# Performance work log

Hardware: AMD Instinct MI355X
Metric: run time of the kernel (lower is better)

The kernel has to match this reference:

```python
import jax, jax.numpy as jnp
import numpy as np

N_EXPERTS = 8
D_MODEL = 1024
D_FF = 2048
NUM_TOKENS = 16384


def setup_inputs() -> dict:
    key = jax.random.key(0)
    k1, k2, k3, k4 = jax.random.split(key, 4)
    x = jax.random.normal(k1, (NUM_TOKENS, D_MODEL), dtype=jnp.float32)
    expert_indices = jax.random.randint(k2, (NUM_TOKENS,), 0, N_EXPERTS, dtype=jnp.int32)
    # init per nn.init.normal_(std=0.02)
    gate_up_weight = 0.02 * jax.random.normal(k3, (N_EXPERTS, 2 * D_FF, D_MODEL), dtype=jnp.float32)
    down_weight = 0.02 * jax.random.normal(k4, (N_EXPERTS, D_MODEL, D_FF), dtype=jnp.float32)
    return {"x": x, "expert_indices": expert_indices,
            "gate_up_weight": gate_up_weight, "down_weight": down_weight}


def reference(x, expert_indices, gate_up_weight, down_weight):
    # Faithful math: each token t uses expert e = expert_indices[t]:
    #   combined = x @ gate_up_weight[e].T ; gate, up = split ; h = silu(gate)*up
    #   out = h @ down_weight[e].T
    # Implemented as a fixed loop over the (small) expert set with masked
    # accumulation, avoiding the original's per-token [2F,D] weight gather.
    n_experts = gate_up_weight.shape[0]
    d_ff = down_weight.shape[2]
    out = jnp.zeros((x.shape[0], down_weight.shape[1]), dtype=x.dtype)
    for e in range(n_experts):
        combined = x @ gate_up_weight[e].T                  # [T, 2*d_ff]
        gate, up = combined[:, :d_ff], combined[:, d_ff:]
        hidden = jax.nn.silu(gate) * up                     # [T, d_ff]
        o = hidden @ down_weight[e].T                       # [T, d_model]
        out = out + jnp.where((expert_indices == e)[:, None], o, 0.0)
    return out
```

## Files before the change

kernel.cpp:

```cpp
#include <hip/hip_runtime.h>

#define NTOK 16384
#define DM 1024
#define DFF 2048
#define NE 8

typedef unsigned short u16;
typedef __attribute__((ext_vector_type(8))) short bf16x8;
typedef __attribute__((ext_vector_type(4))) float f32x4;

__device__ __forceinline__ u16 f2bf(float f) {
  unsigned u = __float_as_uint(f);
  u += 0x7fff + ((u >> 16) & 1);
  return (u16)(u >> 16);
}

__device__ __forceinline__ void async16(const void* g, void* l) {
  __builtin_amdgcn_global_load_lds(
      (const __attribute__((address_space(1))) unsigned int*)g,
      (__attribute__((address_space(3))) unsigned int*)l, 16, 0, 0);
}

__global__ void k_count(const int* __restrict__ idx, int* __restrict__ counts) {
  int t = blockIdx.x * 256 + threadIdx.x;
  atomicAdd(&counts[idx[t]], 1);
}

__global__ void k_offsets(int* __restrict__ c) {
  if (threadIdx.x == 0) {
    int acc = 0;
    for (int e = 0; e < NE; e++) { c[8 + e] = acc; c[16 + e] = acc; acc += c[e]; }
  }
}

__global__ void k_scatter(const int* __restrict__ idx, int* __restrict__ cursor,
                          int* __restrict__ tl) {
  int t = blockIdx.x * 256 + threadIdx.x;
  int pos = atomicAdd(&cursor[idx[t]], 1);
  tl[pos] = t;
}

__global__ void k_cvt_all(const float* __restrict__ x, const float* __restrict__ wgu,
                          const float* __restrict__ wd, u16* __restrict__ xb,
                          u16* __restrict__ wgub, u16* __restrict__ wdb) {
  const size_t N1 = (size_t)NTOK * DM;
  const size_t N2 = (size_t)NE * 2 * DFF * DM;
  const size_t N3 = (size_t)NE * DM * DFF;
  const size_t total4 = (N1 + N2 + N3) / 4;
  for (size_t q = (size_t)blockIdx.x * 256 + threadIdx.x; q < total4;
       q += (size_t)gridDim.x * 256) {
    size_t i = q * 4;
    const float* s;
    u16* d;
    if (i < N1) { s = x + i; d = xb + i; }
    else if (i < N1 + N2) { s = wgu + (i - N1); d = wgub + (i - N1); }
    else { s = wd + (i - N1 - N2); d = wdb + (i - N1 - N2); }
    float4 v = *(const float4*)s;
    ushort4 o;
    o.x = f2bf(v.x); o.y = f2bf(v.y); o.z = f2bf(v.z); o.w = f2bf(v.w);
    *(ushort4*)d = o;
  }
}

__global__ __launch_bounds__(512, 2) void k_gemm1(
    const u16* __restrict__ xb, const u16* __restrict__ wgu,
    u16* __restrict__ hid, const int* __restrict__ tl,
    const int* __restrict__ offs, const int* __restrict__ counts) {
  int wg = blockIdx.x;
  int e = wg & 7;
  int r = wg >> 3;
  int bx = r % 9;
  int by = r / 9;
  int Me = counts[e];
  int m0 = bx * 256;
  if (m0 >= Me) return;
  int n0 = by * 128;
  int oe = offs[e];
  const int* tle = tl + oe;

  int tid = threadIdx.x;
  int lane = tid & 63;
  int wid = tid >> 6;
  int wm = wid >> 2;
  int wn = wid & 3;

  __shared__ u16 lds[2][2][256 * 64];

  int lr = lane >> 3;
  int swz = ((lane & 7) ^ lr) * 8;
  const u16* pA[4];
  const u16* pB[4];
#pragma unroll
  for (int j = 0; j < 4; j++) {
    int c = j * 8 + wid;
    int a = m0 + c * 8 + lr;
    if (a >= Me) a = Me - 1;
    pA[j] = xb + (size_t)tle[a] * DM + swz;
    int b = c * 8 + lr;
    int grow = ((b >> 5) & 1) * DFF + n0 + ((b >> 6) & 3) * 32 + (b & 31);
    pB[j] = wgu + ((size_t)e * 2 * DFF + grow) * DM + swz;
  }

  f32x4 acc[8][4];
#pragma unroll
  for (int m = 0; m < 8; m++)
#pragma unroll
    for (int f = 0; f < 4; f++) acc[m][f] = (f32x4){0.f, 0.f, 0.f, 0.f};

  const int r15 = lane & 15;
  const int hi4 = lane >> 4;
  const int rx = r15 & 7;

#pragma unroll
  for (int j = 0; j < 4; j++) {
    int off = (j * 8 + wid) * 1024;
    async16(pA[j], (char*)&lds[0][0][0] + off);
    async16(pB[j], (char*)&lds[0][1][0] + off);
  }
  asm volatile("s_waitcnt vmcnt(0)" ::: "memory");
  __builtin_amdgcn_s_barrier();
  __builtin_amdgcn_sched_barrier(0);

  int cur = 0;
#pragma unroll 1
  for (int t = 0; t < DM / 64; t++) {
    const char* Ab = (const char*)&lds[cur][0][0];
    const char* Bb = (const char*)&lds[cur][1][0];
    char* LA = (char*)&lds[cur ^ 1][0][0];
    char* LB = (char*)&lds[cur ^ 1][1][0];
    int k1 = (t + 1) * 64;
    bool pf = (t < DM / 64 - 1);
    bf16x8 bfr[4][2];
#pragma unroll
    for (int p = 0; p < 4; p++) {
      if (p == 0) {
#pragma unroll
        for (int f = 0; f < 4; f++)
#pragma unroll
          for (int kk = 0; kk < 2; kk++) {
            int row = wn * 64 + f * 16 + r15;
            bfr[f][kk] = *(const bf16x8*)(Bb + row * 128 + (((kk * 4 + hi4) ^ rx) * 16));
          }
      }
      bf16x8 af[2][2];
#pragma unroll
      for (int i = 0; i < 2; i++)
#pragma unroll
        for (int kk = 0; kk < 2; kk++) {
          int row = wm * 128 + (2 * p + i) * 16 + r15;
          af[i][kk] = *(const bf16x8*)(Ab + row * 128 + (((kk * 4 + hi4) ^ rx) * 16));
        }
      if (pf && p < 2) {
#pragma unroll
        for (int j = 0; j < 2; j++) {
          int jj = p * 2 + j;
          int off = (jj * 8 + wid) * 1024;
          async16(pA[jj] + k1, LA + off);
          async16(pB[jj] + k1, LB + off);
        }
      }
      __builtin_amdgcn_s_barrier();
      __builtin_amdgcn_sched_barrier(0);
      __builtin_amdgcn_s_setprio(1);
#pragma unroll
      for (int kk = 0; kk < 2; kk++)
#pragma unroll
        for (int i = 0; i < 2; i++)
#pragma unroll
          for (int f = 0; f < 4; f++)
            acc[2 * p + i][f] = __builtin_amdgcn_mfma_f32_16x16x32_bf16(
                af[i][kk], bfr[f][kk], acc[2 * p + i][f], 0, 0, 0);
      __builtin_amdgcn_s_setprio(0);
      __builtin_amdgcn_sched_barrier(0);
    }
    asm volatile("s_waitcnt vmcnt(0)" ::: "memory");
    __builtin_amdgcn_s_barrier();
    __builtin_amdgcn_sched_barrier(0);
    cur ^= 1;
  }

  int colb = n0 + wn * 32 + r15;
#pragma unroll
  for (int m = 0; m < 8; m++) {
#pragma unroll
    for (int rr = 0; rr < 4; rr++) {
      int gm = m0 + wm * 128 + m * 16 + hi4 * 4 + rr;
      if (gm < Me) {
        size_t rowp = (size_t)(oe + gm) * DFF;
#pragma unroll
        for (int f = 0; f < 2; f++) {
          float g = acc[m][f][rr];
          float u = acc[m][f + 2][rr];
          float s = g / (1.0f + __expf(-g));
          hid[rowp + colb + f * 16] = f2bf(s * u);
        }
      }
    }
  }
}

__global__ __launch_bounds__(512, 2) void k_gemm2(
    const u16* __restrict__ hid, const u16* __restrict__ wd,
    float* __restrict__ out, const int* __restrict__ tl,
    const int* __restrict__ offs, const int* __restrict__ counts) {
  int wg = blockIdx.x;
  int e = wg & 7;
  int r = wg >> 3;
  int bx = r % 9;
  int by = r / 9;
  int Me = counts[e];
  int m0 = bx * 256;
  if (m0 >= Me) return;
  int n0 = by * 256;
  int oe = offs[e];
  const int* tle = tl + oe;

  int tid = threadIdx.x;
  int lane = tid & 63;
  int wid = tid >> 6;
  int wm = wid >> 2;
  int wn = wid & 3;

  __shared__ u16 lds[2][2][256 * 64];

  int lr = lane >> 3;
  int swz = ((lane & 7) ^ lr) * 8;
  const u16* pA[4];
  const u16* pB[4];
#pragma unroll
  for (int j = 0; j < 4; j++) {
    int c = j * 8 + wid;
    int a = m0 + c * 8 + lr;
    if (a >= Me) a = Me - 1;
    pA[j] = hid + (size_t)(oe + a) * DFF + swz;
    pB[j] = wd + ((size_t)e * DM + n0 + c * 8 + lr) * DFF + swz;
  }

  f32x4 acc[8][4];
#pragma unroll
  for (int m = 0; m < 8; m++)
#pragma unroll
    for (int f = 0; f < 4; f++) acc[m][f] = (f32x4){0.f, 0.f, 0.f, 0.f};

  const int r15 = lane & 15;
  const int hi4 = lane >> 4;
  const int rx = r15 & 7;

#pragma unroll
  for (int j = 0; j < 4; j++) {
    int off = (j * 8 + wid) * 1024;
    async16(pA[j], (char*)&lds[0][0][0] + off);
    async16(pB[j], (char*)&lds[0][1][0] + off);
  }
  asm volatile("s_waitcnt vmcnt(0)" ::: "memory");
  __builtin_amdgcn_s_barrier();
  __builtin_amdgcn_sched_barrier(0);

  int cur = 0;
#pragma unroll 1
  for (int t = 0; t < DFF / 64; t++) {
    const char* Ab = (const char*)&lds[cur][0][0];
    const char* Bb = (const char*)&lds[cur][1][0];
    char* LA = (char*)&lds[cur ^ 1][0][0];
    char* LB = (char*)&lds[cur ^ 1][1][0];
    int k1 = (t + 1) * 64;
    bool pf = (t < DFF / 64 - 1);
    bf16x8 bfr[4][2];
#pragma unroll
    for (int p = 0; p < 4; p++) {
      if (p == 0) {
#pragma unroll
        for (int f = 0; f < 4; f++)
#pragma unroll
          for (int kk = 0; kk < 2; kk++) {
            int row = wn * 64 + f * 16 + r15;
            bfr[f][kk] = *(const bf16x8*)(Bb + row * 128 + (((kk * 4 + hi4) ^ rx) * 16));
          }
      }
      bf16x8 af[2][2];
#pragma unroll
      for (int i = 0; i < 2; i++)
#pragma unroll
        for (int kk = 0; kk < 2; kk++) {
          int row = wm * 128 + (2 * p + i) * 16 + r15;
          af[i][kk] = *(const bf16x8*)(Ab + row * 128 + (((kk * 4 + hi4) ^ rx) * 16));
        }
      if (pf && p < 2) {
#pragma unroll
        for (int j = 0; j < 2; j++) {
          int jj = p * 2 + j;
          int off = (jj * 8 + wid) * 1024;
          async16(pA[jj] + k1, LA + off);
          async16(pB[jj] + k1, LB + off);
        }
      }
      __builtin_amdgcn_s_barrier();
      __builtin_amdgcn_sched_barrier(0);
      __builtin_amdgcn_s_setprio(1);
#pragma unroll
      for (int kk = 0; kk < 2; kk++)
#pragma unroll
        for (int i = 0; i < 2; i++)
#pragma unroll
          for (int f = 0; f < 4; f++)
            acc[2 * p + i][f] = __builtin_amdgcn_mfma_f32_16x16x32_bf16(
                af[i][kk], bfr[f][kk], acc[2 * p + i][f], 0, 0, 0);
      __builtin_amdgcn_s_setprio(0);
      __builtin_amdgcn_sched_barrier(0);
    }
    asm volatile("s_waitcnt vmcnt(0)" ::: "memory");
    __builtin_amdgcn_s_barrier();
    __builtin_amdgcn_sched_barrier(0);
    cur ^= 1;
  }

  int colb = n0 + wn * 64 + r15;
#pragma unroll
  for (int m = 0; m < 8; m++) {
#pragma unroll
    for (int rr = 0; rr < 4; rr++) {
      int gm = m0 + wm * 128 + m * 16 + hi4 * 4 + rr;
      if (gm < Me) {
        int tk = tle[gm];
#pragma unroll
        for (int f = 0; f < 4; f++)
          out[(size_t)tk * DM + colb + f * 16] = acc[m][f][rr];
      }
    }
  }
}

extern "C" void kernel_launch(void* const* d_in, const int* in_sizes, int n_in,
                              void* d_out, int out_size, void* d_ws, size_t ws_size,
                              hipStream_t stream) {
  const float* x   = (const float*)d_in[0];
  const int* eidx  = (const int*)d_in[1];
  const float* wgu = (const float*)d_in[2];
  const float* wd  = (const float*)d_in[3];
  float* out = (float*)d_out;
  char* ws = (char*)d_ws;

  int* ctrl = (int*)ws;
  int* toklist = (int*)(ws + 256);
  u16* xb   = (u16*)(ws + 65792);
  u16* wgub = (u16*)(ws + 65792 + 33554432ull);
  u16* wdb  = (u16*)(ws + 65792 + 33554432ull + 67108864ull);
  u16* hid  = (u16*)(ws + 65792 + 33554432ull + 67108864ull + 33554432ull);

  hipMemsetAsync(ws, 0, 256, stream);
  k_count<<<NTOK / 256, 256, 0, stream>>>(eidx, ctrl);
  k_offsets<<<1, 64, 0, stream>>>(ctrl);
  k_scatter<<<NTOK / 256, 256, 0, stream>>>(eidx, ctrl + 16, toklist);

  k_cvt_all<<<2048, 256, 0, stream>>>(x, wgu, wd, xb, wgub, wdb);

  k_gemm1<<<9 * 16 * NE, 512, 0, stream>>>(xb, wgub, hid, toklist, ctrl + 8, ctrl);
  k_gemm2<<<9 * 4 * NE, 512, 0, stream>>>(hid, wdb, out, toklist, ctrl + 8, ctrl);
}
```

Measured before the change: 470.1 us.

## Restructure LDS tile layout into MFMA-native 16-row chunks with split-K pipelining

```diff
diff --git a/kernel.cpp b/kernel.cpp
--- a/kernel.cpp
+++ b/kernel.cpp
@@ -86,19 +86,19 @@
 
   __shared__ u16 lds[2][2][256 * 64];
 
-  int lr = lane >> 3;
-  int swz = ((lane & 7) ^ lr) * 8;
-  const u16* pA[4];
-  const u16* pB[4];
-#pragma unroll
-  for (int j = 0; j < 4; j++) {
+  int lrc = lane >> 2;
+  int ksl = (lane & 3) * 8;
+  const u16* pA[2];
+  const u16* pB[2];
+#pragma unroll
+  for (int j = 0; j < 2; j++) {
     int c = j * 8 + wid;
-    int a = m0 + c * 8 + lr;
+    int a = m0 + c * 16 + lrc;
     if (a >= Me) a = Me - 1;
-    pA[j] = xb + (size_t)tle[a] * DM + swz;
-    int b = c * 8 + lr;
+    pA[j] = xb + (size_t)tle[a] * DM + ksl;
+    int b = c * 16 + lrc;
     int grow = ((b >> 5) & 1) * DFF + n0 + ((b >> 6) & 3) * 32 + (b & 31);
-    pB[j] = wgu + ((size_t)e * 2 * DFF + grow) * DM + swz;
+    pB[j] = wgu + ((size_t)e * 2 * DFF + grow) * DM + ksl;
   }
 
   f32x4 acc[8][4];
@@ -109,72 +109,117 @@
 
   const int r15 = lane & 15;
   const int hi4 = lane >> 4;
-  const int rx = r15 & 7;
-
-#pragma unroll
-  for (int j = 0; j < 4; j++) {
-    int off = (j * 8 + wid) * 1024;
-    async16(pA[j], (char*)&lds[0][0][0] + off);
-    async16(pB[j], (char*)&lds[0][1][0] + off);
-  }
-  asm volatile("s_waitcnt vmcnt(0)" ::: "memory");
+  const int rb = r15 * 64 + hi4 * 16;
+
+  const int NT = DM / 64;
+
+  {
+    char* LA = (char*)&lds[0][0][0];
+    char* LB = (char*)&lds[0][1][0];
+#pragma unroll
+    for (int j = 0; j < 2; j++) async16(pA[j], LA + (j * 8 + wid) * 2048);
+#pragma unroll
+    for (int j = 0; j < 2; j++) async16(pB[j], LB + (j * 8 + wid) * 2048);
+#pragma unroll
+    for (int j = 0; j < 2; j++) async16(pA[j] + 32, LA + (j * 8 + wid) * 2048 + 1024);
+#pragma unroll
+    for (int j = 0; j < 2; j++) async16(pB[j] + 32, LB + (j * 8 + wid) * 2048 + 1024);
+  }
+  asm volatile("s_waitcnt vmcnt(4)" ::: "memory");
   __builtin_amdgcn_s_barrier();
   __builtin_amdgcn_sched_barrier(0);
 
   int cur = 0;
 #pragma unroll 1
-  for (int t = 0; t < DM / 64; t++) {
+  for (int t = 0; t < NT; t++) {
     const char* Ab = (const char*)&lds[cur][0][0];
     const char* Bb = (const char*)&lds[cur][1][0];
     char* LA = (char*)&lds[cur ^ 1][0][0];
     char* LB = (char*)&lds[cur ^ 1][1][0];
     int k1 = (t + 1) * 64;
-    bool pf = (t < DM / 64 - 1);
-    bf16x8 bfr[4][2];
-#pragma unroll
-    for (int p = 0; p < 4; p++) {
-      if (p == 0) {
-#pragma unroll
-        for (int f = 0; f < 4; f++)
-#pragma unroll
-          for (int kk = 0; kk < 2; kk++) {
-            int row = wn * 64 + f * 16 + r15;
-            bfr[f][kk] = *(const bf16x8*)(Bb + row * 128 + (((kk * 4 + hi4) ^ rx) * 16));
-          }
-      }
-      bf16x8 af[2][2];
-#pragma unroll
-      for (int i = 0; i < 2; i++)
-#pragma unroll
-        for (int kk = 0; kk < 2; kk++) {
-          int row = wm * 128 + (2 * p + i) * 16 + r15;
-          af[i][kk] = *(const bf16x8*)(Ab + row * 128 + (((kk * 4 + hi4) ^ rx) * 16));
-        }
-      if (pf && p < 2) {
-#pragma unroll
-        for (int j = 0; j < 2; j++) {
-          int jj = p * 2 + j;
-          int off = (jj * 8 + wid) * 1024;
-          async16(pA[jj] + k1, LA + off);
-          async16(pB[jj] + k1, LB + off);
-        }
-      }
-      __builtin_amdgcn_s_barrier();
-      __builtin_amdgcn_sched_barrier(0);
-      __builtin_amdgcn_s_setprio(1);
-#pragma unroll
-      for (int kk = 0; kk < 2; kk++)
-#pragma unroll
-        for (int i = 0; i < 2; i++)
-#pragma unroll
-          for (int f = 0; f < 4; f++)
-            acc[2 * p + i][f] = __builtin_amdgcn_mfma_f32_16x16x32_bf16(
-                af[i][kk], bfr[f][kk], acc[2 * p + i][f], 0, 0, 0);
-      __builtin_amdgcn_s_setprio(0);
-      __builtin_amdgcn_sched_barrier(0);
-    }
-    asm volatile("s_waitcnt vmcnt(0)" ::: "memory");
-    __builtin_amdgcn_s_barrier();
+    bool pf = (t + 1 < NT);
+    bf16x8 bfr[4], af[4];
+
+#pragma unroll
+    for (int f = 0; f < 4; f++)
+      bfr[f] = *(const bf16x8*)(Bb + (wn * 4 + f) * 2048 + rb);
+#pragma unroll
+    for (int i = 0; i < 4; i++)
+      af[i] = *(const bf16x8*)(Ab + (wm * 8 + i) * 2048 + rb);
+    if (pf) {
+#pragma unroll
+      for (int j = 0; j < 2; j++) async16(pA[j] + k1, LA + (j * 8 + wid) * 2048);
+    }
+    __builtin_amdgcn_s_barrier();
+    __builtin_amdgcn_sched_barrier(0);
+    __builtin_amdgcn_s_setprio(1);
+#pragma unroll
+    for (int i = 0; i < 4; i++)
+#pragma unroll
+      for (int f = 0; f < 4; f++)
+        acc[i][f] = __builtin_amdgcn_mfma_f32_16x16x32_bf16(af[i], bfr[f], acc[i][f], 0, 0, 0);
+    __builtin_amdgcn_s_setprio(0);
+    __builtin_amdgcn_sched_barrier(0);
+
+#pragma unroll
+    for (int i = 0; i < 4; i++)
+      af[i] = *(const bf16x8*)(Ab + (wm * 8 + 4 + i) * 2048 + rb);
+    if (pf) {
+#pragma unroll
+      for (int j = 0; j < 2; j++) async16(pB[j] + k1, LB + (j * 8 + wid) * 2048);
+      asm volatile("s_waitcnt vmcnt(4)" ::: "memory");
+    } else {
+      asm volatile("s_waitcnt vmcnt(0)" ::: "memory");
+    }
+    __builtin_amdgcn_s_barrier();
+    __builtin_amdgcn_sched_barrier(0);
+    __builtin_amdgcn_s_setprio(1);
+#pragma unroll
+    for (int i = 0; i < 4; i++)
+#pragma unroll
+      for (int f = 0; f < 4; f++)
+        acc[4 + i][f] = __builtin_amdgcn_mfma_f32_16x16x32_bf16(af[i], bfr[f], acc[4 + i][f], 0, 0, 0);
+    __builtin_amdgcn_s_setprio(0);
+    __builtin_amdgcn_sched_barrier(0);
+
+#pragma unroll
+    for (int f = 0; f < 4; f++)
+      bfr[f] = *(const bf16x8*)(Bb + (wn * 4 + f) * 2048 + 1024 + rb);
+#pragma unroll
+    for (int i = 0; i < 4; i++)
+      af[i] = *(const bf16x8*)(Ab + (wm * 8 + i) * 2048 + 1024 + rb);
+    if (pf) {
+#pragma unroll
+      for (int j = 0; j < 2; j++) async16(pA[j] + k1 + 32, LA + (j * 8 + wid) * 2048 + 1024);
+    }
+    __builtin_amdgcn_s_barrier();
+    __builtin_amdgcn_sched_barrier(0);
+    __builtin_amdgcn_s_setprio(1);
+#pragma unroll
+    for (int i = 0; i < 4; i++)
+#pragma unroll
+      for (int f = 0; f < 4; f++)
+        acc[i][f] = __builtin_amdgcn_mfma_f32_16x16x32_bf16(af[i], bfr[f], acc[i][f], 0, 0, 0);
+    __builtin_amdgcn_s_setprio(0);
+    __builtin_amdgcn_sched_barrier(0);
+
+#pragma unroll
+    for (int i = 0; i < 4; i++)
+      af[i] = *(const bf16x8*)(Ab + (wm * 8 + 4 + i) * 2048 + 1024 + rb);
+    if (pf) {
+#pragma unroll
+      for (int j = 0; j < 2; j++) async16(pB[j] + k1 + 32, LB + (j * 8 + wid) * 2048 + 1024);
+      asm volatile("s_waitcnt vmcnt(4)" ::: "memory");
+    }
+    __builtin_amdgcn_s_barrier();
+    __builtin_amdgcn_sched_barrier(0);
+    __builtin_amdgcn_s_setprio(1);
+#pragma unroll
+    for (int i = 0; i < 4; i++)
+#pragma unroll
+      for (int f = 0; f < 4; f++)
+        acc[4 + i][f] = __builtin_amdgcn_mfma_f32_16x16x32_bf16(af[i], bfr[f], acc[4 + i][f], 0, 0, 0);
+    __builtin_amdgcn_s_setprio(0);
     __builtin_amdgcn_sched_barrier(0);
     cur ^= 1;
   }
@@ -223,17 +268,17 @@
 
   __shared__ u16 lds[2][2][256 * 64];
 
-  int lr = lane >> 3;
-  int swz = ((lane & 7) ^ lr) * 8;
-  const u16* pA[4];
-  const u16* pB[4];
-#pragma unroll
-  for (int j = 0; j < 4; j++) {
+  int lrc = lane >> 2;
+  int ksl = (lane & 3) * 8;
+  const u16* pA[2];
+  const u16* pB[2];
+#pragma unroll
+  for (int j = 0; j < 2; j++) {
     int c = j * 8 + wid;
-    int a = m0 + c * 8 + lr;
+    int a = m0 + c * 16 + lrc;
     if (a >= Me) a = Me - 1;
-    pA[j] = hid + (size_t)(oe + a) * DFF + swz;
-    pB[j] = wd + ((size_t)e * DM + n0 + c * 8 + lr) * DFF + swz;
+    pA[j] = hid + (size_t)(oe + a) * DFF + ksl;
+    pB[j] = wd + ((size_t)e * DM + n0 + c * 16 + lrc) * DFF + ksl;
   }
 
   f32x4 acc[8][4];
@@ -244,72 +289,117 @@
 
   const int r15 = lane & 15;
   const int hi4 = lane >> 4;
-  const int rx = r15 & 7;
-
-#pragma unroll
-  for (int j = 0; j < 4; j++) {
-    int off = (j * 8 + wid) * 1024;
-    async16(pA[j], (char*)&lds[0][0][0] + off);
-    async16(pB[j], (char*)&lds[0][1][0] + off);
-  }
-  asm volatile("s_waitcnt vmcnt(0)" ::: "memory");
+  const int rb = r15 * 64 + hi4 * 16;
+
+  const int NT = DFF / 64;
+
+  {
+    char* LA = (char*)&lds[0][0][0];
+    char* LB = (char*)&lds[0][1][0];
+#pragma unroll
+    for (int j = 0; j < 2; j++) async16(pA[j], LA + (j * 8 + wid) * 2048);
+#pragma unroll
+    for (int j = 0; j < 2; j++) async16(pB[j], LB + (j * 8 + wid) * 2048);
+#pragma unroll
+    for (int j = 0; j < 2; j++) async16(pA[j] + 32, LA + (j * 8 + wid) * 2048 + 1024);
+#pragma unroll
+    for (int j = 0; j < 2; j++) async16(pB[j] + 32, LB + (j * 8 + wid) * 2048 + 1024);
+  }
+  asm volatile("s_waitcnt vmcnt(4)" ::: "memory");
   __builtin_amdgcn_s_barrier();
   __builtin_amdgcn_sched_barrier(0);
 
   int cur = 0;
 #pragma unroll 1
-  for (int t = 0; t < DFF / 64; t++) {
+  for (int t = 0; t < NT; t++) {
     const char* Ab = (const char*)&lds[cur][0][0];
     const char* Bb = (const char*)&lds[cur][1][0];
     char* LA = (char*)&lds[cur ^ 1][0][0];
     char* LB = (char*)&lds[cur ^ 1][1][0];
     int k1 = (t + 1) * 64;
-    bool pf = (t < DFF / 64 - 1);
-    bf16x8 bfr[4][2];
-#pragma unroll
-    for (int p = 0; p < 4; p++) {
-      if (p == 0) {
-#pragma unroll
-        for (int f = 0; f < 4; f++)
-#pragma unroll
-          for (int kk = 0; kk < 2; kk++) {
-            int row = wn * 64 + f * 16 + r15;
-            bfr[f][kk] = *(const bf16x8*)(Bb + row * 128 + (((kk * 4 + hi4) ^ rx) * 16));
-          }
-      }
-      bf16x8 af[2][2];
-#pragma unroll
-      for (int i = 0; i < 2; i++)
-#pragma unroll
-        for (int kk = 0; kk < 2; kk++) {
-          int row = wm * 128 + (2 * p + i) * 16 + r15;
-          af[i][kk] = *(const bf16x8*)(Ab + row * 128 + (((kk * 4 + hi4) ^ rx) * 16));
-        }
-      if (pf && p < 2) {
-#pragma unroll
-        for (int j = 0; j < 2; j++) {
-          int jj = p * 2 + j;
-          int off = (jj * 8 + wid) * 1024;
-          async16(pA[jj] + k1, LA + off);
-          async16(pB[jj] + k1, LB + off);
-        }
-      }
-      __builtin_amdgcn_s_barrier();
-      __builtin_amdgcn_sched_barrier(0);
-      __builtin_amdgcn_s_setprio(1);
-#pragma unroll
-      for (int kk = 0; kk < 2; kk++)
-#pragma unroll
-        for (int i = 0; i < 2; i++)
-#pragma unroll
-          for (int f = 0; f < 4; f++)
-            acc[2 * p + i][f] = __builtin_amdgcn_mfma_f32_16x16x32_bf16(
-                af[i][kk], bfr[f][kk], acc[2 * p + i][f], 0, 0, 0);
-      __builtin_amdgcn_s_setprio(0);
-      __builtin_amdgcn_sched_barrier(0);
-    }
-    asm volatile("s_waitcnt vmcnt(0)" ::: "memory");
-    __builtin_amdgcn_s_barrier();
+    bool pf = (t + 1 < NT);
+    bf16x8 bfr[4], af[4];
+
+#pragma unroll
+    for (int f = 0; f < 4; f++)
+      bfr[f] = *(const bf16x8*)(Bb + (wn * 4 + f) * 2048 + rb);
+#pragma unroll
+    for (int i = 0; i < 4; i++)
+      af[i] = *(const bf16x8*)(Ab + (wm * 8 + i) * 2048 + rb);
+    if (pf) {
+#pragma unroll
+      for (int j = 0; j < 2; j++) async16(pA[j] + k1, LA + (j * 8 + wid) * 2048);
+    }
+    __builtin_amdgcn_s_barrier();
+    __builtin_amdgcn_sched_barrier(0);
+    __builtin_amdgcn_s_setprio(1);
+#pragma unroll
+    for (int i = 0; i < 4; i++)
+#pragma unroll
+      for (int f = 0; f < 4; f++)
+        acc[i][f] = __builtin_amdgcn_mfma_f32_16x16x32_bf16(af[i], bfr[f], acc[i][f], 0, 0, 0);
+    __builtin_amdgcn_s_setprio(0);
+    __builtin_amdgcn_sched_barrier(0);
+
+#pragma unroll
+    for (int i = 0; i < 4; i++)
+      af[i] = *(const bf16x8*)(Ab + (wm * 8 + 4 + i) * 2048 + rb);
+    if (pf) {
+#pragma unroll
+      for (int j = 0; j < 2; j++) async16(pB[j] + k1, LB + (j * 8 + wid) * 2048);
+      asm volatile("s_waitcnt vmcnt(4)" ::: "memory");
+    } else {
+      asm volatile("s_waitcnt vmcnt(0)" ::: "memory");
+    }
+    __builtin_amdgcn_s_barrier();
+    __builtin_amdgcn_sched_barrier(0);
+    __builtin_amdgcn_s_setprio(1);
+#pragma unroll
+    for (int i = 0; i < 4; i++)
+#pragma unroll
+      for (int f = 0; f < 4; f++)
+        acc[4 + i][f] = __builtin_amdgcn_mfma_f32_16x16x32_bf16(af[i], bfr[f], acc[4 + i][f], 0, 0, 0);
+    __builtin_amdgcn_s_setprio(0);
+    __builtin_amdgcn_sched_barrier(0);
+
+#pragma unroll
+    for (int f = 0; f < 4; f++)
+      bfr[f] = *(const bf16x8*)(Bb + (wn * 4 + f) * 2048 + 1024 + rb);
+#pragma unroll
+    for (int i = 0; i < 4; i++)
+      af[i] = *(const bf16x8*)(Ab + (wm * 8 + i) * 2048 + 1024 + rb);
+    if (pf) {
+#pragma unroll
+      for (int j = 0; j < 2; j++) async16(pA[j] + k1 + 32, LA + (j * 8 + wid) * 2048 + 1024);
+    }
+    __builtin_amdgcn_s_barrier();
+    __builtin_amdgcn_sched_barrier(0);
+    __builtin_amdgcn_s_setprio(1);
+#pragma unroll
+    for (int i = 0; i < 4; i++)
+#pragma unroll
+      for (int f = 0; f < 4; f++)
+        acc[i][f] = __builtin_amdgcn_mfma_f32_16x16x32_bf16(af[i], bfr[f], acc[i][f], 0, 0, 0);
+    __builtin_amdgcn_s_setprio(0);
+    __builtin_amdgcn_sched_barrier(0);
+
+#pragma unroll
+    for (int i = 0; i < 4; i++)
+      af[i] = *(const bf16x8*)(Ab + (wm * 8 + 4 + i) * 2048 + 1024 + rb);
+    if (pf) {
+#pragma unroll
+      for (int j = 0; j < 2; j++) async16(pB[j] + k1 + 32, LB + (j * 8 + wid) * 2048 + 1024);
+      asm volatile("s_waitcnt vmcnt(4)" ::: "memory");
+    }
+    __builtin_amdgcn_s_barrier();
+    __builtin_amdgcn_sched_barrier(0);
+    __builtin_amdgcn_s_setprio(1);
+#pragma unroll
+    for (int i = 0; i < 4; i++)
+#pragma unroll
+      for (int f = 0; f < 4; f++)
+        acc[4 + i][f] = __builtin_amdgcn_mfma_f32_16x16x32_bf16(af[i], bfr[f], acc[4 + i][f], 0, 0, 0);
+    __builtin_amdgcn_s_setprio(0);
     __builtin_amdgcn_sched_barrier(0);
     cur ^= 1;
   }
```

New measurement: 478.4 us. No clear change (+1.8%).
